# Performance work log

Hardware: AMD Instinct MI355X
Metric: run time of the kernel (lower is better)

## Reference

```python
import jax, jax.numpy as jnp
import numpy as np

N_NODES = 100000
N_EDGES = 3200000
D_IN = 128
D_OUT = 128


def setup_inputs() -> dict:
    key = jax.random.key(0)
    k1, k2, k3, k4, k5, k6 = jax.random.split(key, 6)
    features = jax.random.normal(k1, (N_NODES, D_IN), dtype=jnp.float32)
    norm = jax.random.uniform(k2, (N_EDGES, 1), dtype=jnp.float32)
    src = jax.random.randint(k3, (N_EDGES,), 0, N_NODES)
    dst = jax.random.randint(k4, (N_EDGES,), 0, N_NODES)
    weight = jax.random.normal(k5, (D_OUT, D_IN), dtype=jnp.float32) * (1.0 / np.sqrt(D_IN))
    bias = jax.random.normal(k6, (D_OUT,), dtype=jnp.float32) * 0.01
    return {"features": features, "norm": norm, "src": src, "dst": dst,
            "weight": weight, "bias": bias}


def reference(features, norm, src, dst, weight, bias):
    # message: per-edge gather of src features scaled by edge norm  [E, D_IN]
    msg = norm * features[src]
    # reduce: segment-sum into destination nodes  [N, D_IN]
    h_neigh = jax.ops.segment_sum(msg, dst, num_segments=N_NODES)
    # dense linear (nn.Linear: x @ W^T + b)  [N, D_OUT]
    return h_neigh @ weight.T + bias
```

## Files before the change

kernel.cpp:

```cpp
#include <hip/hip_runtime.h>


#define NN    100000
#define NE    3200000
#define D     128
#define NBKT  391
#define NI4   800000
#define NTILE 6250
#define GB    1563
#define HB    782

typedef __attribute__((ext_vector_type(8))) short bf16x8;
typedef __attribute__((ext_vector_type(4))) float f32x4;

static __device__ __forceinline__ unsigned short f2bf(float x) {
  unsigned u = __float_as_uint(x);
  u += 0x7FFFu + ((u >> 16) & 1u);
  return (unsigned short)(u >> 16);
}

static __device__ __forceinline__ void fmix8(float* acc, uint4 q, float nr) {
  asm("v_fma_mix_f32 %0, %1, %2, %0 op_sel:[0,0,0] op_sel_hi:[1,0,0]"
      : "+v"(acc[0]) : "v"(q.x), "v"(nr));
  asm("v_fma_mix_f32 %0, %1, %2, %0 op_sel:[1,0,0] op_sel_hi:[1,0,0]"
      : "+v"(acc[1]) : "v"(q.x), "v"(nr));
  asm("v_fma_mix_f32 %0, %1, %2, %0 op_sel:[0,0,0] op_sel_hi:[1,0,0]"
      : "+v"(acc[2]) : "v"(q.y), "v"(nr));
  asm("v_fma_mix_f32 %0, %1, %2, %0 op_sel:[1,0,0] op_sel_hi:[1,0,0]"
      : "+v"(acc[3]) : "v"(q.y), "v"(nr));
  asm("v_fma_mix_f32 %0, %1, %2, %0 op_sel:[0,0,0] op_sel_hi:[1,0,0]"
      : "+v"(acc[4]) : "v"(q.z), "v"(nr));
  asm("v_fma_mix_f32 %0, %1, %2, %0 op_sel:[1,0,0] op_sel_hi:[1,0,0]"
      : "+v"(acc[5]) : "v"(q.z), "v"(nr));
  asm("v_fma_mix_f32 %0, %1, %2, %0 op_sel:[0,0,0] op_sel_hi:[1,0,0]"
      : "+v"(acc[6]) : "v"(q.w), "v"(nr));
  asm("v_fma_mix_f32 %0, %1, %2, %0 op_sel:[1,0,0] op_sel_hi:[1,0,0]"
      : "+v"(acc[7]) : "v"(q.w), "v"(nr));
}

__global__ __launch_bounds__(256) void cvtw_kernel(
    const float* __restrict__ w, unsigned short* __restrict__ wfrag) {
  const int i = blockIdx.x * 256 + threadIdx.x;
  const int c = i >> 7, k = i & 127;
  const int pos = ((((c >> 4) << 2) + (k >> 5)) * 64 +
                   (((k >> 3) & 3) << 4) + (c & 15)) * 8 + (k & 7);
  wfrag[pos] = f2bf(w[i]);
}

__global__ __launch_bounds__(256) void gemmhist_kernel(
    const float* __restrict__ f, const unsigned short* __restrict__ wfrag,
    unsigned short* __restrict__ gh, const int* __restrict__ dst,
    int* __restrict__ gcnt) {
  __shared__ int h[4][NBKT];
  if (blockIdx.x >= GB) {
    const int t = threadIdx.x;
    for (int i = t; i < 4 * NBKT; i += 256) ((int*)h)[i] = 0;
    __syncthreads();
    const int i4base = (blockIdx.x - GB) * 1024;
    const int rep = t & 3;
#pragma unroll
    for (int i = 0; i < 4; ++i) {
      const int idx = i4base + i * 256 + t;
      if (idx < NI4) {
        const int4 d = ((const int4*)dst)[idx];
        atomicAdd(&h[rep][d.x >> 8], 1);
        atomicAdd(&h[rep][d.y >> 8], 1);
        atomicAdd(&h[rep][d.z >> 8], 1);
        atomicAdd(&h[rep][d.w >> 8], 1);
      }
    }
    __syncthreads();
    for (int b = t; b < NBKT; b += 256) {
      const int v = h[0][b] + h[1][b] + h[2][b] + h[3][b];
      if (v) atomicAdd(&gcnt[b], v);
    }
    return;
  }

  const int wv = blockIdx.x * 4 + (threadIdx.x >> 6);
  if (wv >= NTILE) return;
  const int lane = threadIdx.x & 63;
  const int mrow = lane & 15;
  const int q = lane >> 4;
  const long node = (long)wv * 16 + mrow;
  const float* fr = f + node * D + q * 8;

  bf16x8 a[4];
#pragma unroll
  for (int ks = 0; ks < 4; ++ks) {
    const float4 lo = *(const float4*)(fr + ks * 32);
    const float4 hi = *(const float4*)(fr + ks * 32 + 4);
    union { bf16x8 v; unsigned short u[8]; } pa;
    pa.u[0] = f2bf(lo.x); pa.u[1] = f2bf(lo.y);
    pa.u[2] = f2bf(lo.z); pa.u[3] = f2bf(lo.w);
    pa.u[4] = f2bf(hi.x); pa.u[5] = f2bf(hi.y);
    pa.u[6] = f2bf(hi.z); pa.u[7] = f2bf(hi.w);
    a[ks] = pa.v;
  }

  const long nbase = (long)wv * 16 + (q << 2);
#pragma unroll
  for (int tc = 0; tc < 8; ++tc) {
    f32x4 acc = {0.f, 0.f, 0.f, 0.f};
#pragma unroll
    for (int ks = 0; ks < 4; ++ks) {
      const bf16x8 b =
          *(const bf16x8*)(wfrag + (((tc << 2) + ks) * 64 + lane) * 8);
      acc = __builtin_amdgcn_mfma_f32_16x16x32_bf16(a[ks], b, acc, 0, 0, 0);
    }
    const int c = (tc << 4) + mrow;
#pragma unroll
    for (int r = 0; r < 4; ++r) {
      union { _Float16 hh; unsigned short u; } cv;
      cv.hh = (_Float16)acc[r];
      gh[(nbase + r) * D + c] = cv.u;
    }
  }
}

__global__ __launch_bounds__(1024) void scan_kernel(const int* __restrict__ gcnt,
                                                    int* __restrict__ bstart,
                                                    int* __restrict__ cur_b,
                                                    int* __restrict__ row_ptr) {
  __shared__ int s[2048];
  const int t = threadIdx.x;
  s[t] = (t < NBKT) ? gcnt[t] : 0;
  s[t + 1024] = 0;
  __syncthreads();
  if (t < 64) {
    int part = 0;
#pragma unroll
    for (int i = 0; i < 32; ++i) part += s[(t << 5) + i];
    int inc = part;
#pragma unroll
    for (int off = 1; off < 64; off <<= 1) {
      int x = __shfl_up(inc, off, 64);
      if (t >= off) inc += x;
    }
    int run = inc - part;
#pragma unroll
    for (int i = 0; i < 32; ++i) {
      int idx = (t << 5) + i;
      int v = s[idx];
      s[idx] = run;
      run += v;
    }
  }
  __syncthreads();
  if (t < NBKT) { bstart[t] = s[t]; cur_b[t] = s[t]; }
  if (t == 0) { bstart[NBKT] = NE; row_ptr[NN] = NE; }
}

__global__ __launch_bounds__(1024) void bin_kernel(
    const int* __restrict__ src, const int* __restrict__ dst,
    const float* __restrict__ norm, int* __restrict__ cur_b,
    int2* __restrict__ bufA) {
  __shared__ int bcnt[4][NBKT];
  __shared__ int bbase[NBKT];
  __shared__ int brank[NBKT];
  const int t = threadIdx.x;
  for (int i = t; i < 4 * NBKT; i += 1024) ((int*)bcnt)[i] = 0;
  if (t < NBKT) brank[t] = 0;
  __syncthreads();
  const int i4base = blockIdx.x * 4096;
  const int rep = t & 3;
#pragma unroll
  for (int i = 0; i < 4; ++i) {
    const int idx = i4base + i * 1024 + t;
    if (idx < NI4) {
      const int4 d = ((const int4*)dst)[idx];
      atomicAdd(&bcnt[rep][d.x >> 8], 1);
      atomicAdd(&bcnt[rep][d.y >> 8], 1);
      atomicAdd(&bcnt[rep][d.z >> 8], 1);
      atomicAdd(&bcnt[rep][d.w >> 8], 1);
    }
  }
  __syncthreads();
  if (t < NBKT) {
    const int c = bcnt[0][t] + bcnt[1][t] + bcnt[2][t] + bcnt[3][t];
    if (c) bbase[t] = atomicAdd(&cur_b[t], c);
  }
  __syncthreads();
#pragma unroll
  for (int i = 0; i < 4; ++i) {
    const int idx = i4base + i * 1024 + t;
    if (idx < NI4) {
      const int4 s = ((const int4*)src)[idx];
      const int4 d = ((const int4*)dst)[idx];
      const float4 nr = ((const float4*)norm)[idx];
      int bb, r; int2 m;
      bb = d.x >> 8; r = atomicAdd(&brank[bb], 1);
      m.x = s.x | ((d.x & 255) << 17); m.y = __float_as_int(nr.x);
      bufA[bbase[bb] + r] = m;
      bb = d.y >> 8; r = atomicAdd(&brank[bb], 1);
      m.x = s.y | ((d.y & 255) << 17); m.y = __float_as_int(nr.y);
      bufA[bbase[bb] + r] = m;
      bb = d.z >> 8; r = atomicAdd(&brank[bb], 1);
      m.x = s.z | ((d.z & 255) << 17); m.y = __float_as_int(nr.z);
      bufA[bbase[bb] + r] = m;
      bb = d.w >> 8; r = atomicAdd(&brank[bb], 1);
      m.x = s.w | ((d.w & 255) << 17); m.y = __float_as_int(nr.w);
      bufA[bbase[bb] + r] = m;
    }
  }
}

__global__ __launch_bounds__(512) void sort_kernel(
    const int2* __restrict__ bufA, const int* __restrict__ bstart,
    int2* __restrict__ bufB, int* __restrict__ row_ptr) {
  __shared__ int lcnt[256];
  __shared__ int lbase[256];
  __shared__ int wtot[4];
  const int b = blockIdx.x;
  const int t = threadIdx.x;
  const int beg = bstart[b];
  const int end = bstart[b + 1];
  if (t < 256) lcnt[t] = 0;
  __syncthreads();
  for (int e = beg + t; e < end; e += 512)
    atomicAdd(&lcnt[(bufA[e].x >> 17) & 255], 1);
  __syncthreads();
  int v = 0, inc = 0;
  const int lane = t & 63;
  if (t < 256) {
    v = lcnt[t];
    inc = v;
#pragma unroll
    for (int off = 1; off < 64; off <<= 1) {
      int x = __shfl_up(inc, off, 64);
      if (lane >= off) inc += x;
    }
    if (lane == 63) wtot[t >> 6] = inc;
  }
  __syncthreads();
  if (t == 0) {
    int run = 0;
#pragma unroll
    for (int i = 0; i < 4; ++i) { int x = wtot[i]; wtot[i] = run; run += x; }
  }
  __syncthreads();
  if (t < 256) {
    const int ex = wtot[t >> 6] + inc - v;
    lbase[t] = ex;
    const int n = (b << 8) + t;
    if (n < NN) row_ptr[n] = beg + ex;
    lcnt[t] = 0;
  }
  __syncthreads();
  for (int e = beg + t; e < end; e += 512) {
    const int2 m = bufA[e];
    const int nl = (m.x >> 17) & 255;
    const int r = atomicAdd(&lcnt[nl], 1);
    int2 o;
    o.x = m.x & 0x1FFFF;
    o.y = m.y;
    bufB[beg + lbase[nl] + r] = o;
  }
}

__global__ __launch_bounds__(256) void pull_kernel(
    const unsigned short* __restrict__ gh, const int* __restrict__ row_ptr,
    const int2* __restrict__ bufB, const float* __restrict__ bias,
    float* __restrict__ out) {
  const int n = blockIdx.x * 4 + (threadIdx.x >> 6);
  if (n >= NN) return;
  const int lane = threadIdx.x & 63;
  const int s = lane & 15;
  const int g = lane >> 4;
  const int beg = row_ptr[n];
  const int end = row_ptr[n + 1];

  float acc[8] = {0.f, 0.f, 0.f, 0.f, 0.f, 0.f, 0.f, 0.f};

  if (beg < end) {
    const char* gbase = (const char*)gh;
    const unsigned soff = (unsigned)(s << 4);
    const int last = end - 1;
    int e0 = beg;
    int2 mA0 = bufB[min(e0 + g, last)];
    int2 mB0 = bufB[min(e0 + 4 + g, last)];
    uint4 qA0 = *(const uint4*)(gbase + (((unsigned)mA0.x << 8) + soff));
    uint4 qB0 = *(const uint4*)(gbase + (((unsigned)mB0.x << 8) + soff));
    int2 mA1 = bufB[min(e0 + 8 + g, last)];
    int2 mB1 = bufB[min(e0 + 12 + g, last)];
    while (e0 + 8 < end) {
      const int2 mA2 = bufB[min(e0 + 16 + g, last)];
      const int2 mB2 = bufB[min(e0 + 20 + g, last)];
      const uint4 qA1 =
          *(const uint4*)(gbase + (((unsigned)mA1.x << 8) + soff));
      const uint4 qB1 =
          *(const uint4*)(gbase + (((unsigned)mB1.x << 8) + soff));
      fmix8(acc, qA0, __int_as_float(mA0.y));
      fmix8(acc, qB0, __int_as_float(mB0.y));
      mA0 = mA1; mB0 = mB1;
      mA1 = mA2; mB1 = mB2;
      qA0 = qA1; qB0 = qB1;
      e0 += 8;
    }
    const float nrA = (e0 + g < end) ? __int_as_float(mA0.y) : 0.f;
    const float nrB = (e0 + 4 + g < end) ? __int_as_float(mB0.y) : 0.f;
    fmix8(acc, qA0, nrA);
    fmix8(acc, qB0, nrB);
  }

#pragma unroll
  for (int k = 0; k < 8; ++k) {
    acc[k] += __shfl_xor(acc[k], 16, 64);
    acc[k] += __shfl_xor(acc[k], 32, 64);
  }
  if (g < 2) {
    const bool hi = (g == 1);
    const float r0 = hi ? acc[4] : acc[0];
    const float r1 = hi ? acc[5] : acc[1];
    const float r2 = hi ? acc[6] : acc[2];
    const float r3 = hi ? acc[7] : acc[3];
    const int cb = (s << 3) + (g << 2);
    const float4 b4 = *(const float4*)(bias + cb);
    float4 r;
    r.x = r0 + b4.x;
    r.y = r1 + b4.y;
    r.z = r2 + b4.z;
    r.w = r3 + b4.w;
    *(float4*)(out + (long)n * D + cb) = r;
  }
}

__global__ __launch_bounds__(256) void gemm_f32_kernel(
    const float* __restrict__ f, const float* __restrict__ w,
    float* __restrict__ g) {
  __shared__ float wlds[D * D];
  const int t = threadIdx.x;
  for (int i = t; i < D * D; i += 256) {
    int c = i >> 7, k = i & 127;
    wlds[(c << 7) + (k ^ (c & 31))] = w[i];
  }
  __syncthreads();
  const int c = t & 127;
  const int cx = c & 31;
  const int cbase = c << 7;
  const int jbase = __builtin_amdgcn_readfirstlane((t >> 7) << 3);
  const long nb = (long)blockIdx.x * 16 + jbase;
  const float* __restrict__ frow = f + nb * D;
  float acc[8] = {0.f, 0.f, 0.f, 0.f, 0.f, 0.f, 0.f, 0.f};
#pragma unroll 4
  for (int k = 0; k < D; ++k) {
    float wv = wlds[cbase + (k ^ cx)];
#pragma unroll
    for (int j = 0; j < 8; ++j) acc[j] += frow[j * D + k] * wv;
  }
#pragma unroll
  for (int j = 0; j < 8; ++j) g[(nb + j) * D + c] = acc[j];
}

__global__ __launch_bounds__(256) void init_kernel(
    const float* __restrict__ bias, float4* __restrict__ out) {
  const int i = blockIdx.x * 256 + threadIdx.x;
  const float4* b4 = (const float4*)bias;
  out[i] = b4[i & 31];
}

__global__ __launch_bounds__(256) void scatter_kernel(
    const float* __restrict__ g, const float* __restrict__ norm,
    const int* __restrict__ src, const int* __restrict__ dst,
    float* __restrict__ out) {
  const long tid = (long)blockIdx.x * 256 + threadIdx.x;
  const int e = (int)(tid >> 5);
  if (e >= NE) return;
  const int ch = (int)(tid & 31) << 2;
  const int s = src[e];
  const int d = dst[e];
  const float nr = norm[e];
  const float4 gv = *(const float4*)(g + (long)s * D + ch);
  float* op = out + (long)d * D + ch;
  unsafeAtomicAdd(op + 0, nr * gv.x);
  unsafeAtomicAdd(op + 1, nr * gv.y);
  unsafeAtomicAdd(op + 2, nr * gv.z);
  unsafeAtomicAdd(op + 3, nr * gv.w);
}

extern "C" void kernel_launch(void* const* d_in, const int* in_sizes, int n_in,
                              void* d_out, int out_size, void* d_ws,
                              size_t ws_size, hipStream_t stream) {
  const float* features = (const float*)d_in[0];
  const float* norm     = (const float*)d_in[1];
  const int*   src      = (const int*)d_in[2];
  const int*   dst      = (const int*)d_in[3];
  const float* weight   = (const float*)d_in[4];
  const float* bias     = (const float*)d_in[5];
  float* out = (float*)d_out;

  char* ws = (char*)d_ws;
  unsigned short* gh    = (unsigned short*)ws;
  int2* bufA    = (int2*)(ws + 25600000);
  int2* bufB    = (int2*)(ws + 51200000);
  int*  row_ptr = (int*)(ws + 76800000);
  int*  gcnt    = (int*)(ws + 77200016);
  int*  bstart  = (int*)(ws + 77201584);
  int*  cur_b   = (int*)(ws + 77203152);
  unsigned short* wfrag = (unsigned short*)(ws + 77204720);
  const size_t need = 77237488;

  if (ws_size >= need) {
    hipMemsetAsync(gcnt, 0, NBKT * sizeof(int), stream);
    hipLaunchKernelGGL(cvtw_kernel, dim3(64), dim3(256), 0, stream,
                       weight, wfrag);
    hipLaunchKernelGGL(gemmhist_kernel, dim3(GB + HB), dim3(256), 0, stream,
                       features, wfrag, gh, dst, gcnt);
    hipLaunchKernelGGL(scan_kernel, dim3(1), dim3(1024), 0, stream,
                       gcnt, bstart, cur_b, row_ptr);
    hipLaunchKernelGGL(bin_kernel, dim3((NI4 + 4095) / 4096), dim3(1024), 0,
                       stream, src, dst, norm, cur_b, bufA);
    hipLaunchKernelGGL(sort_kernel, dim3(NBKT), dim3(512), 0, stream,
                       bufA, bstart, bufB, row_ptr);
    hipLaunchKernelGGL(pull_kernel, dim3((NN + 3) / 4), dim3(256), 0, stream,
                       gh, row_ptr, bufB, bias, out);
  } else {
    float* g = (float*)ws;
    hipLaunchKernelGGL(gemm_f32_kernel, dim3(NN / 16), dim3(256), 0, stream,
                       features, weight, g);
    hipLaunchKernelGGL(init_kernel, dim3((NN * D / 4) / 256), dim3(256), 0,
                       stream, bias, (float4*)out);
    hipLaunchKernelGGL(scatter_kernel, dim3((long)NE * 32 / 256), dim3(256), 0,
                       stream, g, norm, src, dst, out);
  }
}
```

Baseline: 340.6 us.

## Regroup stages: fuse histogram with weight convert, binning with GEMM, deepen pull prefetch

Weight conversion now shares a launch with the destination histogram, and the edge binning pass runs as extra blocks of the GEMM launch, so the memory-bound binning and the MFMA GEMM can overlap. Binning blocks shrink to 256 threads, each handling 16 int4 chunks. The sort kernel moves to 1024 threads per block. The pull kernel's gather pipeline gains one more stage of prefetched edges and features to hide more latency, at the cost of more registers.

```diff
diff --git a/kernel.cpp b/kernel.cpp
--- a/kernel.cpp
+++ b/kernel.cpp
@@ -7,8 +7,9 @@
 #define NBKT  391
 #define NI4   800000
 #define NTILE 6250
+#define HB    782
+#define BB    196
 #define GB    1563
-#define HB    782
 
 typedef __attribute__((ext_vector_type(8))) short bf16x8;
 typedef __attribute__((ext_vector_type(4))) float f32x4;
@@ -38,48 +39,134 @@
       : "+v"(acc[7]) : "v"(q.w), "v"(nr));
 }
 
-__global__ __launch_bounds__(256) void cvtw_kernel(
+__global__ __launch_bounds__(256) void histcvt_kernel(
+    const int* __restrict__ dst, int* __restrict__ gcnt,
     const float* __restrict__ w, unsigned short* __restrict__ wfrag) {
-  const int i = blockIdx.x * 256 + threadIdx.x;
-  const int c = i >> 7, k = i & 127;
-  const int pos = ((((c >> 4) << 2) + (k >> 5)) * 64 +
-                   (((k >> 3) & 3) << 4) + (c & 15)) * 8 + (k & 7);
-  wfrag[pos] = f2bf(w[i]);
-}
-
-__global__ __launch_bounds__(256) void gemmhist_kernel(
-    const float* __restrict__ f, const unsigned short* __restrict__ wfrag,
-    unsigned short* __restrict__ gh, const int* __restrict__ dst,
-    int* __restrict__ gcnt) {
   __shared__ int h[4][NBKT];
-  if (blockIdx.x >= GB) {
-    const int t = threadIdx.x;
-    for (int i = t; i < 4 * NBKT; i += 256) ((int*)h)[i] = 0;
+  const int t = threadIdx.x;
+  if (blockIdx.x >= HB) {
+    const int i = (blockIdx.x - HB) * 256 + t;
+    const int c = i >> 7, k = i & 127;
+    const int pos = ((((c >> 4) << 2) + (k >> 5)) * 64 +
+                     (((k >> 3) & 3) << 4) + (c & 15)) * 8 + (k & 7);
+    wfrag[pos] = f2bf(w[i]);
+    return;
+  }
+  for (int i = t; i < 4 * NBKT; i += 256) ((int*)h)[i] = 0;
+  __syncthreads();
+  const int i4base = blockIdx.x * 1024;
+  const int rep = t & 3;
+#pragma unroll
+  for (int i = 0; i < 4; ++i) {
+    const int idx = i4base + i * 256 + t;
+    if (idx < NI4) {
+      const int4 d = ((const int4*)dst)[idx];
+      atomicAdd(&h[rep][d.x >> 8], 1);
+      atomicAdd(&h[rep][d.y >> 8], 1);
+      atomicAdd(&h[rep][d.z >> 8], 1);
+      atomicAdd(&h[rep][d.w >> 8], 1);
+    }
+  }
+  __syncthreads();
+  for (int b = t; b < NBKT; b += 256) {
+    const int v = h[0][b] + h[1][b] + h[2][b] + h[3][b];
+    if (v) atomicAdd(&gcnt[b], v);
+  }
+}
+
+__global__ __launch_bounds__(1024) void scan_kernel(const int* __restrict__ gcnt,
+                                                    int* __restrict__ bstart,
+                                                    int* __restrict__ cur_b,
+                                                    int* __restrict__ row_ptr) {
+  __shared__ int s[2048];
+  const int t = threadIdx.x;
+  s[t] = (t < NBKT) ? gcnt[t] : 0;
+  s[t + 1024] = 0;
+  __syncthreads();
+  if (t < 64) {
+    int part = 0;
+#pragma unroll
+    for (int i = 0; i < 32; ++i) part += s[(t << 5) + i];
+    int inc = part;
+#pragma unroll
+    for (int off = 1; off < 64; off <<= 1) {
+      int x = __shfl_up(inc, off, 64);
+      if (t >= off) inc += x;
+    }
+    int run = inc - part;
+#pragma unroll
+    for (int i = 0; i < 32; ++i) {
+      int idx = (t << 5) + i;
+      int v = s[idx];
+      s[idx] = run;
+      run += v;
+    }
+  }
+  __syncthreads();
+  if (t < NBKT) { bstart[t] = s[t]; cur_b[t] = s[t]; }
+  if (t == 0) { bstart[NBKT] = NE; row_ptr[NN] = NE; }
+}
+
+__global__ __launch_bounds__(256) void bingemm_kernel(
+    const int* __restrict__ src, const int* __restrict__ dst,
+    const float* __restrict__ norm, int* __restrict__ cur_b,
+    int2* __restrict__ bufA, const float* __restrict__ f,
+    const unsigned short* __restrict__ wfrag, unsigned short* __restrict__ gh) {
+  __shared__ int bcnt[4][NBKT];
+  __shared__ int bbase[NBKT];
+  __shared__ int brank[NBKT];
+  const int t = threadIdx.x;
+  if (blockIdx.x < BB) {
+    for (int i = t; i < 4 * NBKT; i += 256) ((int*)bcnt)[i] = 0;
+    for (int b = t; b < NBKT; b += 256) brank[b] = 0;
     __syncthreads();
-    const int i4base = (blockIdx.x - GB) * 1024;
+    const int i4base = blockIdx.x * 4096;
     const int rep = t & 3;
-#pragma unroll
-    for (int i = 0; i < 4; ++i) {
+#pragma unroll 4
+    for (int i = 0; i < 16; ++i) {
       const int idx = i4base + i * 256 + t;
       if (idx < NI4) {
         const int4 d = ((const int4*)dst)[idx];
-        atomicAdd(&h[rep][d.x >> 8], 1);
-        atomicAdd(&h[rep][d.y >> 8], 1);
-        atomicAdd(&h[rep][d.z >> 8], 1);
-        atomicAdd(&h[rep][d.w >> 8], 1);
+        atomicAdd(&bcnt[rep][d.x >> 8], 1);
+        atomicAdd(&bcnt[rep][d.y >> 8], 1);
+        atomicAdd(&bcnt[rep][d.z >> 8], 1);
+        atomicAdd(&bcnt[rep][d.w >> 8], 1);
       }
     }
     __syncthreads();
     for (int b = t; b < NBKT; b += 256) {
-      const int v = h[0][b] + h[1][b] + h[2][b] + h[3][b];
-      if (v) atomicAdd(&gcnt[b], v);
+      const int c = bcnt[0][b] + bcnt[1][b] + bcnt[2][b] + bcnt[3][b];
+      if (c) bbase[b] = atomicAdd(&cur_b[b], c);
+    }
+    __syncthreads();
+#pragma unroll 4
+    for (int i = 0; i < 16; ++i) {
+      const int idx = i4base + i * 256 + t;
+      if (idx < NI4) {
+        const int4 s = ((const int4*)src)[idx];
+        const int4 d = ((const int4*)dst)[idx];
+        const float4 nr = ((const float4*)norm)[idx];
+        int bb, r; int2 m;
+        bb = d.x >> 8; r = atomicAdd(&brank[bb], 1);
+        m.x = s.x | ((d.x & 255) << 17); m.y = __float_as_int(nr.x);
+        bufA[bbase[bb] + r] = m;
+        bb = d.y >> 8; r = atomicAdd(&brank[bb], 1);
+        m.x = s.y | ((d.y & 255) << 17); m.y = __float_as_int(nr.y);
+        bufA[bbase[bb] + r] = m;
+        bb = d.z >> 8; r = atomicAdd(&brank[bb], 1);
+        m.x = s.z | ((d.z & 255) << 17); m.y = __float_as_int(nr.z);
+        bufA[bbase[bb] + r] = m;
+        bb = d.w >> 8; r = atomicAdd(&brank[bb], 1);
+        m.x = s.w | ((d.w & 255) << 17); m.y = __float_as_int(nr.w);
+        bufA[bbase[bb] + r] = m;
+      }
     }
     return;
   }
 
-  const int wv = blockIdx.x * 4 + (threadIdx.x >> 6);
+  const int wv = (blockIdx.x - BB) * 4 + (t >> 6);
   if (wv >= NTILE) return;
-  const int lane = threadIdx.x & 63;
+  const int lane = t & 63;
   const int mrow = lane & 15;
   const int q = lane >> 4;
   const long node = (long)wv * 16 + mrow;
@@ -118,94 +205,7 @@
   }
 }
 
-__global__ __launch_bounds__(1024) void scan_kernel(const int* __restrict__ gcnt,
-                                                    int* __restrict__ bstart,
-                                                    int* __restrict__ cur_b,
-                                                    int* __restrict__ row_ptr) {
-  __shared__ int s[2048];
-  const int t = threadIdx.x;
-  s[t] = (t < NBKT) ? gcnt[t] : 0;
-  s[t + 1024] = 0;
-  __syncthreads();
-  if (t < 64) {
-    int part = 0;
-#pragma unroll
-    for (int i = 0; i < 32; ++i) part += s[(t << 5) + i];
-    int inc = part;
-#pragma unroll
-    for (int off = 1; off < 64; off <<= 1) {
-      int x = __shfl_up(inc, off, 64);
-      if (t >= off) inc += x;
-    }
-    int run = inc - part;
-#pragma unroll
-    for (int i = 0; i < 32; ++i) {
-      int idx = (t << 5) + i;
-      int v = s[idx];
-      s[idx] = run;
-      run += v;
-    }
-  }
-  __syncthreads();
-  if (t < NBKT) { bstart[t] = s[t]; cur_b[t] = s[t]; }
-  if (t == 0) { bstart[NBKT] = NE; row_ptr[NN] = NE; }
-}
-
-__global__ __launch_bounds__(1024) void bin_kernel(
-    const int* __restrict__ src, const int* __restrict__ dst,
-    const float* __restrict__ norm, int* __restrict__ cur_b,
-    int2* __restrict__ bufA) {
-  __shared__ int bcnt[4][NBKT];
-  __shared__ int bbase[NBKT];
-  __shared__ int brank[NBKT];
-  const int t = threadIdx.x;
-  for (int i = t; i < 4 * NBKT; i += 1024) ((int*)bcnt)[i] = 0;
-  if (t < NBKT) brank[t] = 0;
-  __syncthreads();
-  const int i4base = blockIdx.x * 4096;
-  const int rep = t & 3;
-#pragma unroll
-  for (int i = 0; i < 4; ++i) {
-    const int idx = i4base + i * 1024 + t;
-    if (idx < NI4) {
-      const int4 d = ((const int4*)dst)[idx];
-      atomicAdd(&bcnt[rep][d.x >> 8], 1);
-      atomicAdd(&bcnt[rep][d.y >> 8], 1);
-      atomicAdd(&bcnt[rep][d.z >> 8], 1);
-      atomicAdd(&bcnt[rep][d.w >> 8], 1);
-    }
-  }
-  __syncthreads();
-  if (t < NBKT) {
-    const int c = bcnt[0][t] + bcnt[1][t] + bcnt[2][t] + bcnt[3][t];
-    if (c) bbase[t] = atomicAdd(&cur_b[t], c);
-  }
-  __syncthreads();
-#pragma unroll
-  for (int i = 0; i < 4; ++i) {
-    const int idx = i4base + i * 1024 + t;
-    if (idx < NI4) {
-      const int4 s = ((const int4*)src)[idx];
-      const int4 d = ((const int4*)dst)[idx];
-      const float4 nr = ((const float4*)norm)[idx];
-      int bb, r; int2 m;
-      bb = d.x >> 8; r = atomicAdd(&brank[bb], 1);
-      m.x = s.x | ((d.x & 255) << 17); m.y = __float_as_int(nr.x);
-      bufA[bbase[bb] + r] = m;
-      bb = d.y >> 8; r = atomicAdd(&brank[bb], 1);
-      m.x = s.y | ((d.y & 255) << 17); m.y = __float_as_int(nr.y);
-      bufA[bbase[bb] + r] = m;
-      bb = d.z >> 8; r = atomicAdd(&brank[bb], 1);
-      m.x = s.z | ((d.z & 255) << 17); m.y = __float_as_int(nr.z);
-      bufA[bbase[bb] + r] = m;
-      bb = d.w >> 8; r = atomicAdd(&brank[bb], 1);
-      m.x = s.w | ((d.w & 255) << 17); m.y = __float_as_int(nr.w);
-      bufA[bbase[bb] + r] = m;
-    }
-  }
-}
-
-__global__ __launch_bounds__(512) void sort_kernel(
+__global__ __launch_bounds__(1024) void sort_kernel(
     const int2* __restrict__ bufA, const int* __restrict__ bstart,
     int2* __restrict__ bufB, int* __restrict__ row_ptr) {
   __shared__ int lcnt[256];
@@ -217,7 +217,7 @@
   const int end = bstart[b + 1];
   if (t < 256) lcnt[t] = 0;
   __syncthreads();
-  for (int e = beg + t; e < end; e += 512)
+  for (int e = beg + t; e < end; e += 1024)
     atomicAdd(&lcnt[(bufA[e].x >> 17) & 255], 1);
   __syncthreads();
   int v = 0, inc = 0;
@@ -247,7 +247,7 @@
     lcnt[t] = 0;
   }
   __syncthreads();
-  for (int e = beg + t; e < end; e += 512) {
+  for (int e = beg + t; e < end; e += 1024) {
     const int2 m = bufA[e];
     const int nl = (m.x >> 17) & 255;
     const int r = atomicAdd(&lcnt[nl], 1);
@@ -279,28 +279,42 @@
     int e0 = beg;
     int2 mA0 = bufB[min(e0 + g, last)];
     int2 mB0 = bufB[min(e0 + 4 + g, last)];
+    int2 mA1 = bufB[min(e0 + 8 + g, last)];
+    int2 mB1 = bufB[min(e0 + 12 + g, last)];
+    int2 mA2 = bufB[min(e0 + 16 + g, last)];
+    int2 mB2 = bufB[min(e0 + 20 + g, last)];
     uint4 qA0 = *(const uint4*)(gbase + (((unsigned)mA0.x << 8) + soff));
     uint4 qB0 = *(const uint4*)(gbase + (((unsigned)mB0.x << 8) + soff));
-    int2 mA1 = bufB[min(e0 + 8 + g, last)];
-    int2 mB1 = bufB[min(e0 + 12 + g, last)];
-    while (e0 + 8 < end) {
-      const int2 mA2 = bufB[min(e0 + 16 + g, last)];
-      const int2 mB2 = bufB[min(e0 + 20 + g, last)];
-      const uint4 qA1 =
-          *(const uint4*)(gbase + (((unsigned)mA1.x << 8) + soff));
-      const uint4 qB1 =
-          *(const uint4*)(gbase + (((unsigned)mB1.x << 8) + soff));
+    uint4 qA1 = *(const uint4*)(gbase + (((unsigned)mA1.x << 8) + soff));
+    uint4 qB1 = *(const uint4*)(gbase + (((unsigned)mB1.x << 8) + soff));
+    while (e0 + 16 < end) {
+      const int2 mA3 = bufB[min(e0 + 24 + g, last)];
+      const int2 mB3 = bufB[min(e0 + 28 + g, last)];
+      const uint4 qA2 =
+          *(const uint4*)(gbase + (((unsigned)mA2.x << 8) + soff));
+      const uint4 qB2 =
+          *(const uint4*)(gbase + (((unsigned)mB2.x << 8) + soff));
       fmix8(acc, qA0, __int_as_float(mA0.y));
       fmix8(acc, qB0, __int_as_float(mB0.y));
       mA0 = mA1; mB0 = mB1;
       mA1 = mA2; mB1 = mB2;
+      mA2 = mA3; mB2 = mB3;
       qA0 = qA1; qB0 = qB1;
+      qA1 = qA2; qB1 = qB2;
       e0 += 8;
     }
-    const float nrA = (e0 + g < end) ? __int_as_float(mA0.y) : 0.f;
-    const float nrB = (e0 + 4 + g < end) ? __int_as_float(mB0.y) : 0.f;
-    fmix8(acc, qA0, nrA);
-    fmix8(acc, qB0, nrB);
+    {
+      const float nrA = (e0 + g < end) ? __int_as_float(mA0.y) : 0.f;
+      const float nrB = (e0 + 4 + g < end) ? __int_as_float(mB0.y) : 0.f;
+      fmix8(acc, qA0, nrA);
+      fmix8(acc, qB0, nrB);
+    }
+    {
+      const float nrA = (e0 + 8 + g < end) ? __int_as_float(mA1.y) : 0.f;
+      const float nrB = (e0 + 12 + g < end) ? __int_as_float(mB1.y) : 0.f;
+      fmix8(acc, qA1, nrA);
+      fmix8(acc, qB1, nrB);
+    }
   }
 
 #pragma unroll
@@ -402,15 +416,13 @@
 
   if (ws_size >= need) {
     hipMemsetAsync(gcnt, 0, NBKT * sizeof(int), stream);
-    hipLaunchKernelGGL(cvtw_kernel, dim3(64), dim3(256), 0, stream,
-                       weight, wfrag);
-    hipLaunchKernelGGL(gemmhist_kernel, dim3(GB + HB), dim3(256), 0, stream,
-                       features, wfrag, gh, dst, gcnt);
+    hipLaunchKernelGGL(histcvt_kernel, dim3(HB + 64), dim3(256), 0, stream,
+                       dst, gcnt, weight, wfrag);
     hipLaunchKernelGGL(scan_kernel, dim3(1), dim3(1024), 0, stream,
                        gcnt, bstart, cur_b, row_ptr);
-    hipLaunchKernelGGL(bin_kernel, dim3((NI4 + 4095) / 4096), dim3(1024), 0,
-                       stream, src, dst, norm, cur_b, bufA);
-    hipLaunchKernelGGL(sort_kernel, dim3(NBKT), dim3(512), 0, stream,
+    hipLaunchKernelGGL(bingemm_kernel, dim3(BB + GB), dim3(256), 0, stream,
+                       src, dst, norm, cur_b, bufA, features, wfrag, gh);
+    hipLaunchKernelGGL(sort_kernel, dim3(NBKT), dim3(1024), 0, stream,
                        bufA, bstart, bufB, row_ptr);
     hipLaunchKernelGGL(pull_kernel, dim3((NN + 3) / 4), dim3(256), 0, stream,
                        gh, row_ptr, bufB, bias, out);
```

Measured after the change: 361.0 us. 6.0% more time.

## Move dense GEMM from histogram kernel into the sort kernel launch

Applied to the files above, without the earlier changes.

The weight conversion is merged with the dst histogram into one launch, and the feature×weight bf16 MFMA GEMM moves from that launch into the per-bucket sort kernel as extra blocks. The 391 sort blocks are few and latency-bound, so the GEMM blocks can fill idle CUs during the sort. The change also removes one launch (cvtw). The GEMM now uses 512-thread blocks with 8 waves each. The risk is that the GEMM's memory traffic competes with the sort's scattered writes.

```diff
diff --git a/kernel.cpp b/kernel.cpp
--- a/kernel.cpp
+++ b/kernel.cpp
@@ -7,8 +7,8 @@
 #define NBKT  391
 #define NI4   800000
 #define NTILE 6250
-#define GB    1563
 #define HB    782
+#define GB2   782
 
 typedef __attribute__((ext_vector_type(8))) short bf16x8;
 typedef __attribute__((ext_vector_type(4))) float f32x4;
@@ -38,83 +38,38 @@
       : "+v"(acc[7]) : "v"(q.w), "v"(nr));
 }
 
-__global__ __launch_bounds__(256) void cvtw_kernel(
+__global__ __launch_bounds__(256) void histcvt_kernel(
+    const int* __restrict__ dst, int* __restrict__ gcnt,
     const float* __restrict__ w, unsigned short* __restrict__ wfrag) {
-  const int i = blockIdx.x * 256 + threadIdx.x;
-  const int c = i >> 7, k = i & 127;
-  const int pos = ((((c >> 4) << 2) + (k >> 5)) * 64 +
-                   (((k >> 3) & 3) << 4) + (c & 15)) * 8 + (k & 7);
-  wfrag[pos] = f2bf(w[i]);
-}
-
-__global__ __launch_bounds__(256) void gemmhist_kernel(
-    const float* __restrict__ f, const unsigned short* __restrict__ wfrag,
-    unsigned short* __restrict__ gh, const int* __restrict__ dst,
-    int* __restrict__ gcnt) {
   __shared__ int h[4][NBKT];
-  if (blockIdx.x >= GB) {
-    const int t = threadIdx.x;
-    for (int i = t; i < 4 * NBKT; i += 256) ((int*)h)[i] = 0;
-    __syncthreads();
-    const int i4base = (blockIdx.x - GB) * 1024;
-    const int rep = t & 3;
-#pragma unroll
-    for (int i = 0; i < 4; ++i) {
-      const int idx = i4base + i * 256 + t;
-      if (idx < NI4) {
-        const int4 d = ((const int4*)dst)[idx];
-        atomicAdd(&h[rep][d.x >> 8], 1);
-        atomicAdd(&h[rep][d.y >> 8], 1);
-        atomicAdd(&h[rep][d.z >> 8], 1);
-        atomicAdd(&h[rep][d.w >> 8], 1);
-      }
-    }
-    __syncthreads();
-    for (int b = t; b < NBKT; b += 256) {
-      const int v = h[0][b] + h[1][b] + h[2][b] + h[3][b];
-      if (v) atomicAdd(&gcnt[b], v);
-    }
+  const int t = threadIdx.x;
+  if (blockIdx.x >= HB) {
+    const int i = (blockIdx.x - HB) * 256 + t;
+    const int c = i >> 7, k = i & 127;
+    const int pos = ((((c >> 4) << 2) + (k >> 5)) * 64 +
+                     (((k >> 3) & 3) << 4) + (c & 15)) * 8 + (k & 7);
+    wfrag[pos] = f2bf(w[i]);
     return;
   }
-
-  const int wv = blockIdx.x * 4 + (threadIdx.x >> 6);
-  if (wv >= NTILE) return;
-  const int lane = threadIdx.x & 63;
-  const int mrow = lane & 15;
-  const int q = lane >> 4;
-  const long node = (long)wv * 16 + mrow;
-  const float* fr = f + node * D + q * 8;
-
-  bf16x8 a[4];
-#pragma unroll
-  for (int ks = 0; ks < 4; ++ks) {
-    const float4 lo = *(const float4*)(fr + ks * 32);
-    const float4 hi = *(const float4*)(fr + ks * 32 + 4);
-    union { bf16x8 v; unsigned short u[8]; } pa;
-    pa.u[0] = f2bf(lo.x); pa.u[1] = f2bf(lo.y);
-    pa.u[2] = f2bf(lo.z); pa.u[3] = f2bf(lo.w);
-    pa.u[4] = f2bf(hi.x); pa.u[5] = f2bf(hi.y);
-    pa.u[6] = f2bf(hi.z); pa.u[7] = f2bf(hi.w);
-    a[ks] = pa.v;
-  }
-
-  const long nbase = (long)wv * 16 + (q << 2);
-#pragma unroll
-  for (int tc = 0; tc < 8; ++tc) {
-    f32x4 acc = {0.f, 0.f, 0.f, 0.f};
-#pragma unroll
-    for (int ks = 0; ks < 4; ++ks) {
-      const bf16x8 b =
-          *(const bf16x8*)(wfrag + (((tc << 2) + ks) * 64 + lane) * 8);
-      acc = __builtin_amdgcn_mfma_f32_16x16x32_bf16(a[ks], b, acc, 0, 0, 0);
-    }
-    const int c = (tc << 4) + mrow;
-#pragma unroll
-    for (int r = 0; r < 4; ++r) {
-      union { _Float16 hh; unsigned short u; } cv;
-      cv.hh = (_Float16)acc[r];
-      gh[(nbase + r) * D + c] = cv.u;
-    }
+  for (int i = t; i < 4 * NBKT; i += 256) ((int*)h)[i] = 0;
+  __syncthreads();
+  const int i4base = blockIdx.x * 1024;
+  const int rep = t & 3;
+#pragma unroll
+  for (int i = 0; i < 4; ++i) {
+    const int idx = i4base + i * 256 + t;
+    if (idx < NI4) {
+      const int4 d = ((const int4*)dst)[idx];
+      atomicAdd(&h[rep][d.x >> 8], 1);
+      atomicAdd(&h[rep][d.y >> 8], 1);
+      atomicAdd(&h[rep][d.z >> 8], 1);
+      atomicAdd(&h[rep][d.w >> 8], 1);
+    }
+  }
+  __syncthreads();
+  for (int b = t; b < NBKT; b += 256) {
+    const int v = h[0][b] + h[1][b] + h[2][b] + h[3][b];
+    if (v) atomicAdd(&gcnt[b], v);
   }
 }
 
@@ -205,56 +160,101 @@
   }
 }
 
-__global__ __launch_bounds__(512) void sort_kernel(
+__global__ __launch_bounds__(512) void sortgemm_kernel(
     const int2* __restrict__ bufA, const int* __restrict__ bstart,
-    int2* __restrict__ bufB, int* __restrict__ row_ptr) {
+    int2* __restrict__ bufB, int* __restrict__ row_ptr,
+    const float* __restrict__ f, const unsigned short* __restrict__ wfrag,
+    unsigned short* __restrict__ gh) {
   __shared__ int lcnt[256];
   __shared__ int lbase[256];
   __shared__ int wtot[4];
-  const int b = blockIdx.x;
   const int t = threadIdx.x;
-  const int beg = bstart[b];
-  const int end = bstart[b + 1];
-  if (t < 256) lcnt[t] = 0;
-  __syncthreads();
-  for (int e = beg + t; e < end; e += 512)
-    atomicAdd(&lcnt[(bufA[e].x >> 17) & 255], 1);
-  __syncthreads();
-  int v = 0, inc = 0;
+  if (blockIdx.x < NBKT) {
+    const int b = blockIdx.x;
+    const int beg = bstart[b];
+    const int end = bstart[b + 1];
+    if (t < 256) lcnt[t] = 0;
+    __syncthreads();
+    for (int e = beg + t; e < end; e += 512)
+      atomicAdd(&lcnt[(bufA[e].x >> 17) & 255], 1);
+    __syncthreads();
+    int v = 0, inc = 0;
+    const int lane = t & 63;
+    if (t < 256) {
+      v = lcnt[t];
+      inc = v;
+#pragma unroll
+      for (int off = 1; off < 64; off <<= 1) {
+        int x = __shfl_up(inc, off, 64);
+        if (lane >= off) inc += x;
+      }
+      if (lane == 63) wtot[t >> 6] = inc;
+    }
+    __syncthreads();
+    if (t == 0) {
+      int run = 0;
+#pragma unroll
+      for (int i = 0; i < 4; ++i) { int x = wtot[i]; wtot[i] = run; run += x; }
+    }
+    __syncthreads();
+    if (t < 256) {
+      const int ex = wtot[t >> 6] + inc - v;
+      lbase[t] = ex;
+      const int n = (b << 8) + t;
+      if (n < NN) row_ptr[n] = beg + ex;
+      lcnt[t] = 0;
+    }
+    __syncthreads();
+    for (int e = beg + t; e < end; e += 512) {
+      const int2 m = bufA[e];
+      const int nl = (m.x >> 17) & 255;
+      const int r = atomicAdd(&lcnt[nl], 1);
+      int2 o;
+      o.x = m.x & 0x1FFFF;
+      o.y = m.y;
+      bufB[beg + lbase[nl] + r] = o;
+    }
+    return;
+  }
+
+  const int wv = (blockIdx.x - NBKT) * 8 + (t >> 6);
+  if (wv >= NTILE) return;
   const int lane = t & 63;
-  if (t < 256) {
-    v = lcnt[t];
-    inc = v;
-#pragma unroll
-    for (int off = 1; off < 64; off <<= 1) {
-      int x = __shfl_up(inc, off, 64);
-      if (lane >= off) inc += x;
-    }
-    if (lane == 63) wtot[t >> 6] = inc;
-  }
-  __syncthreads();
-  if (t == 0) {
-    int run = 0;
-#pragma unroll
-    for (int i = 0; i < 4; ++i) { int x = wtot[i]; wtot[i] = run; run += x; }
-  }
-  __syncthreads();
-  if (t < 256) {
-    const int ex = wtot[t >> 6] + inc - v;
-    lbase[t] = ex;
-    const int n = (b << 8) + t;
-    if (n < NN) row_ptr[n] = beg + ex;
-    lcnt[t] = 0;
-  }
-  __syncthreads();
-  for (int e = beg + t; e < end; e += 512) {
-    const int2 m = bufA[e];
-    const int nl = (m.x >> 17) & 255;
-    const int r = atomicAdd(&lcnt[nl], 1);
-    int2 o;
-    o.x = m.x & 0x1FFFF;
-    o.y = m.y;
-    bufB[beg + lbase[nl] + r] = o;
+  const int mrow = lane & 15;
+  const int q = lane >> 4;
+  const long node = (long)wv * 16 + mrow;
+  const float* fr = f + node * D + q * 8;
+
+  bf16x8 a[4];
+#pragma unroll
+  for (int ks = 0; ks < 4; ++ks) {
+    const float4 lo = *(const float4*)(fr + ks * 32);
+    const float4 hi = *(const float4*)(fr + ks * 32 + 4);
+    union { bf16x8 v; unsigned short u[8]; } pa;
+    pa.u[0] = f2bf(lo.x); pa.u[1] = f2bf(lo.y);
+    pa.u[2] = f2bf(lo.z); pa.u[3] = f2bf(lo.w);
+    pa.u[4] = f2bf(hi.x); pa.u[5] = f2bf(hi.y);
+    pa.u[6] = f2bf(hi.z); pa.u[7] = f2bf(hi.w);
+    a[ks] = pa.v;
+  }
+
+  const long nbase = (long)wv * 16 + (q << 2);
+#pragma unroll
+  for (int tc = 0; tc < 8; ++tc) {
+    f32x4 acc = {0.f, 0.f, 0.f, 0.f};
+#pragma unroll
+    for (int ks = 0; ks < 4; ++ks) {
+      const bf16x8 b =
+          *(const bf16x8*)(wfrag + (((tc << 2) + ks) * 64 + lane) * 8);
+      acc = __builtin_amdgcn_mfma_f32_16x16x32_bf16(a[ks], b, acc, 0, 0, 0);
+    }
+    const int c = (tc << 4) + mrow;
+#pragma unroll
+    for (int r = 0; r < 4; ++r) {
+      union { _Float16 hh; unsigned short u; } cv;
+      cv.hh = (_Float16)acc[r];
+      gh[(nbase + r) * D + c] = cv.u;
+    }
   }
 }
 
@@ -402,16 +402,14 @@
 
   if (ws_size >= need) {
     hipMemsetAsync(gcnt, 0, NBKT * sizeof(int), stream);
-    hipLaunchKernelGGL(cvtw_kernel, dim3(64), dim3(256), 0, stream,
-                       weight, wfrag);
-    hipLaunchKernelGGL(gemmhist_kernel, dim3(GB + HB), dim3(256), 0, stream,
-                       features, wfrag, gh, dst, gcnt);
+    hipLaunchKernelGGL(histcvt_kernel, dim3(HB + 64), dim3(256), 0, stream,
+                       dst, gcnt, weight, wfrag);
     hipLaunchKernelGGL(scan_kernel, dim3(1), dim3(1024), 0, stream,
                        gcnt, bstart, cur_b, row_ptr);
     hipLaunchKernelGGL(bin_kernel, dim3((NI4 + 4095) / 4096), dim3(1024), 0,
                        stream, src, dst, norm, cur_b, bufA);
-    hipLaunchKernelGGL(sort_kernel, dim3(NBKT), dim3(512), 0, stream,
-                       bufA, bstart, bufB, row_ptr);
+    hipLaunchKernelGGL(sortgemm_kernel, dim3(NBKT + GB2), dim3(512), 0, stream,
+                       bufA, bstart, bufB, row_ptr, features, wfrag, gh);
     hipLaunchKernelGGL(pull_kernel, dim3((NN + 3) / 4), dim3(256), 0, stream,
                        gh, row_ptr, bufB, bias, out);
   } else {
```

Result: no change. 343.9 us (+1.0%).
